# Kernel tuning notes

Measured on AMD Instinct MI355X. Metric: run time of the kernel, lower is better.

The kernel has to match this reference:

```python
import jax, jax.numpy as jnp
import numpy as np

IMG = 1536
STRIDES = [8, 16, 32, 64, 128]
SCALES = np.array([2.0 ** 0, 2.0 ** (1.0 / 3.0), 2.0 ** (2.0 / 3.0)])
RATIOS = np.array([0.5, 1.0, 2.0])
THRESHOLD = 0.5
IOU_THRESHOLD = 0.5
N_KEEP = 1000  # fixed candidate budget for jit-compatible NMS


def make_anchors():
    """Multi-level RetinaNet-style anchors in (x1, y1, x2, y2), [A, 4]."""
    all_boxes = []
    for s in STRIDES:
        base = 4.0 * s
        fs = IMG // s
        areas = (base * SCALES) ** 2
        ws, hs = [], []
        for r in RATIOS:
            ws.append(np.sqrt(areas / r))
            hs.append(np.sqrt(areas * r))
        ws = np.concatenate(ws)  # [9]
        hs = np.concatenate(hs)
        cx = (np.arange(fs) + 0.5) * s
        cy = (np.arange(fs) + 0.5) * s
        cxg, cyg = np.meshgrid(cx, cy)
        cxg = cxg.reshape(-1, 1)
        cyg = cyg.reshape(-1, 1)
        boxes = np.stack([cxg - ws / 2, cyg - hs / 2, cxg + ws / 2, cyg + hs / 2], axis=-1)
        all_boxes.append(boxes.reshape(-1, 4))
    return np.concatenate(all_boxes, axis=0).astype(np.float32)


def setup_inputs() -> dict:
    key = jax.random.key(0)
    k1, k2 = jax.random.split(key)
    anchors = jnp.asarray(make_anchors())  # [441936, 4]
    A = anchors.shape[0]
    cla = jax.random.uniform(k1, (1, A, 80), dtype=jnp.float32)  # sigmoid-like class scores
    reg = 0.1 * jax.random.normal(k2, (1, A, 4), dtype=jnp.float32)  # box deltas
    return {"cla": cla, "reg": reg, "anchors": anchors, "height": IMG, "width": IMG}


def decode_box(anchors, deltas):
    wa = anchors[:, 2] - anchors[:, 0]
    ha = anchors[:, 3] - anchors[:, 1]
    cxa = anchors[:, 0] + 0.5 * wa
    cya = anchors[:, 1] + 0.5 * ha
    cx = cxa + deltas[:, 0] * wa
    cy = cya + deltas[:, 1] * ha
    w = wa * jnp.exp(deltas[:, 2])
    h = ha * jnp.exp(deltas[:, 3])
    return jnp.stack([cx - 0.5 * w, cy - 0.5 * h, cx + 0.5 * w, cy + 0.5 * h], axis=-1)


def iou_matrix(b):
    x1 = jnp.maximum(b[:, None, 0], b[None, :, 0])
    y1 = jnp.maximum(b[:, None, 1], b[None, :, 1])
    x2 = jnp.minimum(b[:, None, 2], b[None, :, 2])
    y2 = jnp.minimum(b[:, None, 3], b[None, :, 3])
    inter = jnp.clip(x2 - x1, 0.0) * jnp.clip(y2 - y1, 0.0)
    area = jnp.clip(b[:, 2] - b[:, 0], 0.0) * jnp.clip(b[:, 3] - b[:, 1], 0.0)
    union = area[:, None] + area[None, :] - inter
    return inter / jnp.maximum(union, 1e-8)


def reference(cla, reg, anchors, height, width):
    # decode + clip (clipbox)
    boxes = decode_box(anchors, reg[0])  # [A, 4]
    boxes = jnp.stack([
        jnp.clip(boxes[:, 0], 0.0, width - 1.0),
        jnp.clip(boxes[:, 1], 0.0, height - 1.0),
        jnp.clip(boxes[:, 2], 0.0, width - 1.0),
        jnp.clip(boxes[:, 3], 0.0, height - 1.0),
    ], axis=-1)
    # per-anchor best class score (torch.max over dim=2)
    scores_all = jnp.max(cla[0], axis=1)  # [A]
    # fixed-size candidate set replaces data-dependent boolean masking
    top_scores, idx = jax.lax.top_k(scores_all, N_KEEP)
    cand_boxes = boxes[idx]            # [N, 4]
    cand_cla = cla[0][idx]             # [N, C]
    valid = top_scores > THRESHOLD     # score thresholding
    iou = iou_matrix(cand_boxes)       # [N, N]

    def body(i, keep):
        suppressed = jnp.any(keep & (iou[i] > IOU_THRESHOLD))
        return keep.at[i].set(valid[i] & ~suppressed)

    keep = jax.lax.fori_loop(0, N_KEEP, body, jnp.zeros((N_KEEP,), dtype=bool))

    nms_scores = jnp.where(keep, jnp.max(cand_cla, axis=1), 0.0)
    nms_class = jnp.where(keep, jnp.argmax(cand_cla, axis=1), -1)
    nms_boxes = jnp.where(keep[:, None], cand_boxes, 0.0)
    return nms_scores, nms_class, nms_boxes
```

## Files before the change

kernel.cpp:

```cpp
#include <hip/hip_runtime.h>
#include <stdint.h>


#define NK 1000
#define CAP 2048
#define NS 1024
#define NCLS 80
#define NW 16
typedef unsigned long long ull;

static inline __device__ unsigned fkey(float f) {
  unsigned u = __float_as_uint(f);
  return (u & 0x80000000u) ? ~u : (u | 0x80000000u);
}
static inline __device__ float fkey_inv(unsigned k) {
  unsigned u = (k & 0x80000000u) ? (k & 0x7fffffffu) : ~k;
  return __uint_as_float(u);
}

__device__ __forceinline__ void scan_select(const unsigned* __restrict__ gh, int nbins,
                                            unsigned k, unsigned* s_sum, unsigned* s_res,
                                            unsigned& digit, unsigned& cum_above) {
  int t = threadIdx.x;
  int chunk = nbins >> 8;
  if (chunk < 1) chunk = 1;
  int base = t * chunk;
  unsigned s = 0;
  if (t < 256)
    for (int b = 0; b < chunk; ++b) s += gh[base + b];
  if (t < 256) s_sum[t] = s;
  __syncthreads();
  if (t < 256) {
    unsigned ca = 0;
    for (int u = t + 1; u < 256; ++u) ca += s_sum[u];
    if (ca < k && ca + s >= k) {
      unsigned cum = ca;
      for (int b = chunk - 1; b >= 0; --b) {
        unsigned c = gh[base + b];
        if (cum + c >= k) { s_res[0] = (unsigned)(base + b); s_res[1] = cum; break; }
        cum += c;
      }
    }
  }
  __syncthreads();
  digit = s_res[0];
  cum_above = s_res[1];
  __syncthreads();
}

__global__ __launch_bounds__(256) void k_score(const float* __restrict__ cla,
                                               unsigned* __restrict__ keys,
                                               unsigned* __restrict__ hist0,
                                               uint4* __restrict__ zreg, int nz4,
                                               int A) {
  __shared__ unsigned lh[4096];
  int t = threadIdx.x;
  {
    const uint4 z = make_uint4(0u, 0u, 0u, 0u);
    int stride = gridDim.x * 256;
    for (int i = blockIdx.x * 256 + t; i < nz4; i += stride) zreg[i] = z;
  }
  for (int i = t; i < 4096; i += 256) lh[i] = 0u;
  __syncthreads();
  const int lane = t & 63, wib = t >> 6;
  const int gwave = blockIdx.x * 4 + wib, nwaves = gridDim.x * 4;
  const int q = lane >> 2, sub = lane & 3;
  const int ntask = (A + 15) >> 4;
  for (int task = gwave; task < ntask; task += nwaves) {
    int a = task * 16 + q;
    float m = -3.402823466e38f;
    if (a < A) {
      const float4* p = (const float4*)(cla + (size_t)a * NCLS);
#pragma unroll
      for (int j = 0; j < 5; ++j) {
        float4 v = p[sub + j * 4];
        m = fmaxf(m, fmaxf(fmaxf(v.x, v.y), fmaxf(v.z, v.w)));
      }
    }
    m = fmaxf(m, __shfl_xor(m, 1, 64));
    m = fmaxf(m, __shfl_xor(m, 2, 64));
    if (sub == 0 && a < A) {
      unsigned key = fkey(m);
      keys[a] = key;
      atomicAdd(&lh[key >> 20], 1u);
    }
  }
  __syncthreads();
  for (int i = t; i < 4096; i += 256) {
    unsigned c = lh[i];
    if (c) atomicAdd(&hist0[i], c);
  }
}

__global__ __launch_bounds__(256) void k_hist1(const unsigned* __restrict__ keys,
                                               const unsigned* __restrict__ hist0,
                                               unsigned* __restrict__ leaf,
                                               unsigned* __restrict__ summary, int A) {
  __shared__ unsigned lh[4096];
  __shared__ unsigned s_sum[256];
  __shared__ unsigned s_res[2];
  int t = threadIdx.x;
  unsigned d0, ca;
  scan_select(hist0, 4096, NK, s_sum, s_res, d0, ca);
  for (int i = t; i < 4096; i += 256) lh[i] = 0u;
  __syncthreads();
  int tid = blockIdx.x * 256 + t, nthr = gridDim.x * 256;
  for (int a = tid; a < A; a += nthr) {
    unsigned key = keys[a];
    if ((key >> 20) == d0) {
      unsigned low = key & 0xFFFFFu;
      atomicAdd(&leaf[low], 1u);
      atomicAdd(&lh[low >> 8], 1u);
    }
  }
  __syncthreads();
  for (int i = t; i < 4096; i += 256) {
    unsigned c = lh[i];
    if (c) atomicAdd(&summary[i], c);
  }
}

__global__ __launch_bounds__(256) void k_gather(const unsigned* __restrict__ keys,
                                                const unsigned* __restrict__ hist0,
                                                const unsigned* __restrict__ leaf,
                                                const unsigned* __restrict__ summary,
                                                unsigned* __restrict__ meta,
                                                ull* __restrict__ cand_keys, int A) {
  __shared__ unsigned s_sum[256];
  __shared__ unsigned s_res[2];
  __shared__ ull lbuf[1024];
  __shared__ unsigned lcnt;
  __shared__ unsigned gbase;
  int t = threadIdx.x;
  unsigned k_rem = NK, d0, g, b, ca;
  scan_select(hist0, 4096, k_rem, s_sum, s_res, d0, ca);
  k_rem -= ca;
  scan_select(summary, 4096, k_rem, s_sum, s_res, g, ca);
  k_rem -= ca;
  scan_select(leaf + (size_t)g * 256, 256, k_rem, s_sum, s_res, b, ca);
  const unsigned T = (d0 << 20) | (g << 8) | b;
  if (t == 0) lcnt = 0u;
  __syncthreads();
  int tid = blockIdx.x * 256 + t, nthr = gridDim.x * 256;
  for (int a = tid; a < A; a += nthr) {
    unsigned key = keys[a];
    if (key >= T) {
      unsigned pos = atomicAdd(&lcnt, 1u);
      if (pos < 1024)
        lbuf[pos] = ((ull)key << 32) | (ull)(~(unsigned)a);
    }
  }
  __syncthreads();
  if (t == 0) gbase = (lcnt > 0) ? atomicAdd(&meta[0], lcnt) : 0u;
  __syncthreads();
  unsigned n = lcnt < 1024u ? lcnt : 1024u;
  for (unsigned i = t; i < n; i += 256) {
    unsigned pos = gbase + i;
    if (pos < CAP) cand_keys[pos] = lbuf[i];
  }
}

__global__ __launch_bounds__(1024) void k_supdec(
    const float* __restrict__ cla, const float* __restrict__ reg,
    const float* __restrict__ anchors, const int* __restrict__ hp,
    const int* __restrict__ wp, const ull* __restrict__ cand_keys,
    ull* __restrict__ sup, unsigned* __restrict__ meta,
    float* __restrict__ out) {
  __shared__ ull ckl[NS];
  __shared__ float4 bx[NS];
  __shared__ float ar[NS];
  __shared__ unsigned keptm[32], notm[32];
  __shared__ int s_chg;
  __shared__ int s_last;
  int t = threadIdx.x;
  ckl[t] = cand_keys[t];
  __syncthreads();
  ull ck = ckl[t];
  float score = 0.0f;
  bool valid = false;
  if (ck != 0ull) {
    unsigned a = ~(unsigned)(ck & 0xFFFFFFFFull);
    score = fkey_inv((unsigned)(ck >> 32));
    float W1 = (float)wp[0] - 1.0f;
    float H1 = (float)hp[0] - 1.0f;
    float4 dd = ((const float4*)reg)[a];
    float4 an = ((const float4*)anchors)[a];
    float wa = an.z - an.x, ha = an.w - an.y;
    float cxa = an.x + 0.5f * wa, cya = an.y + 0.5f * ha;
    float cx = cxa + dd.x * wa, cy = cya + dd.y * ha;
    float w = wa * expf(dd.z), h = ha * expf(dd.w);
    float x1 = fminf(fmaxf(cx - 0.5f * w, 0.0f), W1);
    float y1 = fminf(fmaxf(cy - 0.5f * h, 0.0f), H1);
    float x2 = fminf(fmaxf(cx + 0.5f * w, 0.0f), W1);
    float y2 = fminf(fmaxf(cy + 0.5f * h, 0.0f), H1);
    bx[t] = make_float4(x1, y1, x2, y2);
    ar[t] = fmaxf(x2 - x1, 0.0f) * fmaxf(y2 - y1, 0.0f);
    valid = (score > 0.5f);
  } else {
    bx[t] = make_float4(0.f, 0.f, 0.f, 0.f);
    ar[t] = 0.0f;
  }
  __syncthreads();
  {
    int gidx = blockIdx.x * 1024 + t;
    int i = gidx >> 4, w = gidx & 15;
    ull cki = ckl[i];
    float4 bi = bx[i];
    float ai = ar[i];
    ull bits = 0ull;
    int j0 = w * 64;
#pragma unroll 4
    for (int s = 0; s < 64; ++s) {
      int jj = (s + w) & 63;
      int j = j0 + jj;
      ull ckj = ckl[j];
      if (ckj > cki) {
        float4 bj = bx[j];
        float xx1 = fmaxf(bi.x, bj.x), yy1 = fmaxf(bi.y, bj.y);
        float xx2 = fminf(bi.z, bj.z), yy2 = fminf(bi.w, bj.w);
        float inter = fmaxf(xx2 - xx1, 0.0f) * fmaxf(yy2 - yy1, 0.0f);
        float uni = ai + ar[j] - inter;
        float iou = inter / fmaxf(uni, 1e-8f);
        if (iou > 0.5f) bits |= (1ull << jj);
      }
    }
    sup[(size_t)i * NW + w] = bits;
  }
  __threadfence();
  __syncthreads();
  if (t == 0) {
    unsigned done = __hip_atomic_fetch_add(&meta[1], 1u, __ATOMIC_ACQ_REL,
                                           __HIP_MEMORY_SCOPE_AGENT);
    s_last = (done == gridDim.x - 1) ? 1 : 0;
    s_chg = 0;
  }
  __syncthreads();
  if (!s_last) return;
  unsigned rnk = 0;
  for (int j = 0; j < NS; ++j) rnk += (ckl[j] > ck) ? 1u : 0u;
  if (t < 32) { keptm[t] = 0u; notm[t] = 0u; }
  bool active = (ck != 0ull) && (rnk < NK);
  bool decided = (!active) || (!valid);
  ull rw[NW];
#pragma unroll
  for (int w = 0; w < NW; ++w)
    rw[w] = __hip_atomic_load(&sup[(size_t)t * NW + w], __ATOMIC_RELAXED,
                              __HIP_MEMORY_SCOPE_AGENT);
  __syncthreads();
  if (decided) atomicOr(&notm[t >> 5], 1u << (t & 31));
  __syncthreads();
  for (int round = 0; round < NS; ++round) {
    if (!decided) {
      ull hit = 0ull, pot = 0ull;
#pragma unroll
      for (int w = 0; w < NW; ++w) {
        ull km = ((ull)keptm[2 * w + 1] << 32) | (ull)keptm[2 * w];
        ull nm = ((ull)notm[2 * w + 1] << 32) | (ull)notm[2 * w];
        hit |= rw[w] & km;
        pot |= rw[w] & ~(km | nm);
      }
      if (hit) {
        decided = true;
        atomicOr(&notm[t >> 5], 1u << (t & 31));
        s_chg = 1;
      } else if (!pot) {
        decided = true;
        atomicOr(&keptm[t >> 5], 1u << (t & 31));
        s_chg = 1;
      }
    }
    __syncthreads();
    if (s_chg == 0) break;
    __syncthreads();
    if (t == 0) s_chg = 0;
    __syncthreads();
  }
  if (active) {
    bool kp = (keptm[t >> 5] >> (t & 31)) & 1u;
    int ci = 0;
    if (kp) {
      unsigned a = ~(unsigned)(ck & 0xFFFFFFFFull);
      const float* row = cla + (size_t)a * NCLS;
      float m = -3.402823466e38f;
#pragma unroll
      for (int j = 0; j < NCLS; ++j) {
        float v = row[j];
        if (v > m) { m = v; ci = j; }
      }
    }
    out[rnk] = kp ? score : 0.0f;
    out[NK + rnk] = kp ? (float)ci : -1.0f;
    float4 bo = bx[t];
    ((float4*)(out + 2 * NK))[rnk] = kp ? bo : make_float4(0.f, 0.f, 0.f, 0.f);
  }
}

extern "C" void kernel_launch(void* const* d_in, const int* in_sizes, int n_in,
                              void* d_out, int out_size, void* d_ws, size_t ws_size,
                              hipStream_t stream) {
  const float* cla = (const float*)d_in[0];
  const float* reg = (const float*)d_in[1];
  const float* anchors = (const float*)d_in[2];
  const int* hp = (const int*)d_in[3];
  const int* wp = (const int*)d_in[4];
  float* out = (float*)d_out;
  int A = in_sizes[2] / 4;

  char* ws = (char*)d_ws;
  size_t off = 0;
  auto carve = [&](size_t bytes) -> void* {
    void* p = ws + off;
    off += bytes;
    off = (off + 255) & ~(size_t)255;
    return p;
  };
  unsigned* keys = (unsigned*)carve((size_t)A * 4);
  unsigned* hist0 = (unsigned*)carve(4096 * 4);
  char* zbase = ws + off;
  unsigned* leaf = (unsigned*)carve((size_t)(1 << 20) * 4);
  unsigned* summary = (unsigned*)carve(4096 * 4);
  unsigned* meta = (unsigned*)carve(2 * 4);
  ull* cand_keys = (ull*)carve(CAP * 8);
  size_t zbytes = (size_t)((ws + off) - zbase);
  int nz4 = (int)(zbytes / 16);
  ull* sup = (ull*)carve((size_t)NS * NW * 8);
  (void)ws_size;
  (void)n_in;
  (void)out_size;

  hipMemsetAsync(hist0, 0, 4096 * 4, stream);
  k_score<<<1024, 256, 0, stream>>>(cla, keys, hist0, (uint4*)zbase, nz4, A);
  k_hist1<<<512, 256, 0, stream>>>(keys, hist0, leaf, summary, A);
  k_gather<<<512, 256, 0, stream>>>(keys, hist0, leaf, summary, meta, cand_keys, A);
  k_supdec<<<16, 1024, 0, stream>>>(cla, reg, anchors, hp, wp, cand_keys, sup, meta,
                                    out);
}
```

Baseline: 313.9 us.

## Fuse candidate gather into suppression kernel with per-thread compaction

Removes the separate gather kernel and its global-atomic candidate buffer. Each of the 16 suppression blocks now recomputes the threshold selection itself and scans all keys with vectorized uint4 loads. Each thread keeps up to 12 hits in registers, and a wave shuffle prefix sum places them into shared memory in a deterministic order. This saves a launch and a global round-trip, at the cost of every block redundantly reading the whole key array. It would also silently drop candidates if one thread's strided slice held more than 12 keys above the threshold.

```diff
diff --git a/kernel.cpp b/kernel.cpp
--- a/kernel.cpp
+++ b/kernel.cpp
@@ -3,10 +3,10 @@
 
 
 #define NK 1000
-#define CAP 2048
 #define NS 1024
 #define NCLS 80
 #define NW 16
+#define HCAP 12
 typedef unsigned long long ull;
 
 static inline __device__ unsigned fkey(float f) {
@@ -120,17 +120,22 @@
   }
 }
 
-__global__ __launch_bounds__(256) void k_gather(const unsigned* __restrict__ keys,
-                                                const unsigned* __restrict__ hist0,
-                                                const unsigned* __restrict__ leaf,
-                                                const unsigned* __restrict__ summary,
-                                                unsigned* __restrict__ meta,
-                                                ull* __restrict__ cand_keys, int A) {
+__global__ __launch_bounds__(1024) void k_supdec(
+    const float* __restrict__ cla, const float* __restrict__ reg,
+    const float* __restrict__ anchors, const int* __restrict__ hp,
+    const int* __restrict__ wp, const unsigned* __restrict__ keys,
+    const unsigned* __restrict__ hist0, const unsigned* __restrict__ leaf,
+    const unsigned* __restrict__ summary, ull* __restrict__ sup,
+    unsigned* __restrict__ meta, float* __restrict__ out, int A) {
   __shared__ unsigned s_sum[256];
   __shared__ unsigned s_res[2];
-  __shared__ ull lbuf[1024];
-  __shared__ unsigned lcnt;
-  __shared__ unsigned gbase;
+  __shared__ ull ckl[NS];
+  __shared__ float4 bx[NS];
+  __shared__ float ar[NS];
+  __shared__ unsigned wsum[16];
+  __shared__ unsigned keptm[32], notm[32];
+  __shared__ int s_chg;
+  __shared__ int s_last;
   int t = threadIdx.x;
   unsigned k_rem = NK, d0, g, b, ca;
   scan_select(hist0, 4096, k_rem, s_sum, s_res, d0, ca);
@@ -139,41 +144,41 @@
   k_rem -= ca;
   scan_select(leaf + (size_t)g * 256, 256, k_rem, s_sum, s_res, b, ca);
   const unsigned T = (d0 << 20) | (g << 8) | b;
-  if (t == 0) lcnt = 0u;
-  __syncthreads();
-  int tid = blockIdx.x * 256 + t, nthr = gridDim.x * 256;
-  for (int a = tid; a < A; a += nthr) {
-    unsigned key = keys[a];
-    if (key >= T) {
-      unsigned pos = atomicAdd(&lcnt, 1u);
-      if (pos < 1024)
-        lbuf[pos] = ((ull)key << 32) | (ull)(~(unsigned)a);
-    }
-  }
-  __syncthreads();
-  if (t == 0) gbase = (lcnt > 0) ? atomicAdd(&meta[0], lcnt) : 0u;
-  __syncthreads();
-  unsigned n = lcnt < 1024u ? lcnt : 1024u;
-  for (unsigned i = t; i < n; i += 256) {
-    unsigned pos = gbase + i;
-    if (pos < CAP) cand_keys[pos] = lbuf[i];
-  }
-}
-
-__global__ __launch_bounds__(1024) void k_supdec(
-    const float* __restrict__ cla, const float* __restrict__ reg,
-    const float* __restrict__ anchors, const int* __restrict__ hp,
-    const int* __restrict__ wp, const ull* __restrict__ cand_keys,
-    ull* __restrict__ sup, unsigned* __restrict__ meta,
-    float* __restrict__ out) {
-  __shared__ ull ckl[NS];
-  __shared__ float4 bx[NS];
-  __shared__ float ar[NS];
-  __shared__ unsigned keptm[32], notm[32];
-  __shared__ int s_chg;
-  __shared__ int s_last;
-  int t = threadIdx.x;
-  ckl[t] = cand_keys[t];
+  ckl[t] = 0ull;
+  unsigned ha[HCAP];
+  unsigned hc = 0;
+  int nv = A >> 2;
+  const uint4* k4 = (const uint4*)keys;
+  for (int i = t; i < nv; i += 1024) {
+    uint4 v = k4[i];
+    if (v.x >= T && hc < HCAP) ha[hc++] = (unsigned)(4 * i);
+    if (v.y >= T && hc < HCAP) ha[hc++] = (unsigned)(4 * i + 1);
+    if (v.z >= T && hc < HCAP) ha[hc++] = (unsigned)(4 * i + 2);
+    if (v.w >= T && hc < HCAP) ha[hc++] = (unsigned)(4 * i + 3);
+  }
+  for (int a2 = (nv << 2) + t; a2 < A; a2 += 1024) {
+    if (keys[a2] >= T && hc < HCAP) ha[hc++] = (unsigned)a2;
+  }
+  {
+    int lane = t & 63, w = t >> 6;
+    unsigned v = hc;
+    for (int off = 1; off < 64; off <<= 1) {
+      unsigned u = __shfl_up(v, off, 64);
+      if (lane >= off) v += u;
+    }
+    if (lane == 63) wsum[w] = v;
+    __syncthreads();
+    unsigned wo = 0;
+    for (int j = 0; j < w; ++j) wo += wsum[j];
+    unsigned base = wo + v - hc;
+    for (unsigned q = 0; q < hc; ++q) {
+      unsigned pos = base + q;
+      if (pos < NS) {
+        unsigned a = ha[q];
+        ckl[pos] = ((ull)keys[a] << 32) | (ull)(~a);
+      }
+    }
+  }
   __syncthreads();
   ull ck = ckl[t];
   float score = 0.0f;
@@ -185,10 +190,10 @@
     float H1 = (float)hp[0] - 1.0f;
     float4 dd = ((const float4*)reg)[a];
     float4 an = ((const float4*)anchors)[a];
-    float wa = an.z - an.x, ha = an.w - an.y;
-    float cxa = an.x + 0.5f * wa, cya = an.y + 0.5f * ha;
-    float cx = cxa + dd.x * wa, cy = cya + dd.y * ha;
-    float w = wa * expf(dd.z), h = ha * expf(dd.w);
+    float wa = an.z - an.x, haa = an.w - an.y;
+    float cxa = an.x + 0.5f * wa, cya = an.y + 0.5f * haa;
+    float cx = cxa + dd.x * wa, cy = cya + dd.y * haa;
+    float w = wa * expf(dd.z), h = haa * expf(dd.w);
     float x1 = fminf(fmaxf(cx - 0.5f * w, 0.0f), W1);
     float y1 = fminf(fmaxf(cy - 0.5f * h, 0.0f), H1);
     float x2 = fminf(fmaxf(cx + 0.5f * w, 0.0f), W1);
@@ -319,8 +324,7 @@
   char* zbase = ws + off;
   unsigned* leaf = (unsigned*)carve((size_t)(1 << 20) * 4);
   unsigned* summary = (unsigned*)carve(4096 * 4);
-  unsigned* meta = (unsigned*)carve(2 * 4);
-  ull* cand_keys = (ull*)carve(CAP * 8);
+  unsigned* meta = (unsigned*)carve(8 * 4);
   size_t zbytes = (size_t)((ws + off) - zbase);
   int nz4 = (int)(zbytes / 16);
   ull* sup = (ull*)carve((size_t)NS * NW * 8);
@@ -331,7 +335,6 @@
   hipMemsetAsync(hist0, 0, 4096 * 4, stream);
   k_score<<<1024, 256, 0, stream>>>(cla, keys, hist0, (uint4*)zbase, nz4, A);
   k_hist1<<<512, 256, 0, stream>>>(keys, hist0, leaf, summary, A);
-  k_gather<<<512, 256, 0, stream>>>(keys, hist0, leaf, summary, meta, cand_keys, A);
-  k_supdec<<<16, 1024, 0, stream>>>(cla, reg, anchors, hp, wp, cand_keys, sup, meta,
-                                    out);
-}
+  k_supdec<<<16, 1024, 0, stream>>>(cla, reg, anchors, hp, wp, keys, hist0, leaf,
+                                    summary, sup, meta, out, A);
+}
```

Result: slower. 418.1 us (+33.2%).
